# Optimization experiments

Measured on AMD Instinct MI355X. Metric: run time of the kernel, lower is better.

The kernel has to match this reference:

```python
import jax, jax.numpy as jnp
import numpy as np

N = 100000        # nodes
E = 1600000       # edges (avg degree 16)
IN_C = 128
HID = 128
OUT_C = 18


def setup_inputs() -> dict:
    key = jax.random.key(0)
    k_x, k_e, k_w1, k_b1, k_w2, k_b2 = jax.random.split(key, 6)
    x = jax.random.normal(k_x, (N, IN_C), dtype=jnp.float32)
    edge_index = jax.random.randint(k_e, (2, E), 0, N, dtype=jnp.int64)
    # Glorot-ish init for linear weights, zero bias (PyG GCNConv defaults)
    W1 = jax.random.normal(k_w1, (IN_C, HID), dtype=jnp.float32) / np.sqrt(IN_C)
    b1 = jnp.zeros((HID,), dtype=jnp.float32)
    W2 = jax.random.normal(k_w2, (HID, OUT_C), dtype=jnp.float32) / np.sqrt(HID)
    b2 = jnp.zeros((OUT_C,), dtype=jnp.float32)
    return {"x": x, "edge_index": edge_index, "W1": W1, "b1": b1, "W2": W2, "b2": b2}


def _gcn_conv(x, src, dst, norm, W, b, n_nodes):
    # PyG GCNConv: linear transform, then normalized scatter-add aggregation
    h = x @ W                                   # [N, d_out]
    msg = h[src] * norm[:, None]                # gather + scale: [E+N, d_out]
    out = jax.ops.segment_sum(msg, dst, num_segments=n_nodes)
    return out + b


def reference(x, edge_index, W1, b1, W2, b2):
    src, dst = edge_index[0], edge_index[1]
    loop = jnp.arange(N, dtype=edge_index.dtype)
    src_f = jnp.concatenate([src, loop])        # add self-loops
    dst_f = jnp.concatenate([dst, loop])
    # symmetric normalization deg^-1/2[src] * deg^-1/2[dst] (with self-loops)
    deg = jax.ops.segment_sum(jnp.ones_like(dst_f, dtype=x.dtype), dst_f, num_segments=N)
    dinv = jnp.where(deg > 0, jax.lax.rsqrt(deg), 0.0)
    norm = dinv[src_f] * dinv[dst_f]            # [E+N]

    h = _gcn_conv(x, src_f, dst_f, norm, W1, b1, N)
    h = jax.nn.relu(h)
    # dropout is identity in eval mode (training=False)
    h = _gcn_conv(h, src_f, dst_f, norm, W2, b2, N)
    return jax.nn.log_softmax(h, axis=1)
```

## Files before the change

kernel.cpp:

```cpp
#include <hip/hip_runtime.h>
#include <math.h>

#define NN 100000
#define NE 1600000
#define CH  128
#define CO  18
#define NPB 256
#define NBUK ((NN + NPB - 1) / NPB)
#define EPB 4096
#define NBB ((NE + EPB - 1) / EPB)

typedef unsigned int uint;
typedef unsigned short ushort;
typedef float floatx4 __attribute__((ext_vector_type(4)));
typedef short short8 __attribute__((ext_vector_type(8)));
typedef ushort ushort4v __attribute__((ext_vector_type(4)));

__device__ __forceinline__ float bf_lo(uint u) { return __uint_as_float(u << 16); }
__device__ __forceinline__ float bf_hi(uint u) { return __uint_as_float(u & 0xFFFF0000u); }
__device__ __forceinline__ ushort f2bf(float f) {
    uint u = __float_as_uint(f);
    u += 0x7FFFu + ((u >> 16) & 1u);
    return (ushort)(u >> 16);
}
__device__ __forceinline__ uint pack_bf16(float a, float b) {
    return (uint)f2bf(a) | ((uint)f2bf(b) << 16);
}


__global__ __launch_bounds__(256) void k_bhist(const int* __restrict__ dst,
                                               int* __restrict__ bcnt) {
    __shared__ int h[NBUK];
    int tid = threadIdx.x;
    for (int i = tid; i < NBUK; i += 256) h[i] = 0;
    __syncthreads();
    int e0 = blockIdx.x * EPB;
#pragma unroll
    for (int i = 0; i < EPB / 256; ++i) {
        int e = e0 + i * 256 + tid;
        if (e < NE) atomicAdd(&h[dst[e] >> 8], 1);
    }
    __syncthreads();
    for (int i = tid; i < NBUK; i += 256)
        if (h[i]) atomicAdd(&bcnt[i], h[i]);
}

__global__ __launch_bounds__(512) void k_bscan(const int* __restrict__ bcnt,
                                               int* __restrict__ bbase,
                                               int* __restrict__ bcur) {
    __shared__ int s[512];
    int tid = threadIdx.x;
    int c = (tid < NBUK) ? bcnt[tid] : 0;
    s[tid] = c;
    __syncthreads();
    for (int off = 1; off < 512; off <<= 1) {
        int t = (tid >= off) ? s[tid - off] : 0;
        __syncthreads();
        s[tid] += t;
        __syncthreads();
    }
    if (tid < NBUK) {
        int ex = s[tid] - c;
        bbase[tid] = ex;
        bcur[tid] = ex;
    }
    if (tid == NBUK) bbase[NBUK] = NE;
}

__global__ __launch_bounds__(256) void k_bin(const int* __restrict__ src,
                                             const int* __restrict__ dst,
                                             int* __restrict__ bcur,
                                             uint2* __restrict__ etmp) {
    __shared__ int h[NBUK];
    __shared__ int base[NBUK];
    int tid = threadIdx.x;
    for (int i = tid; i < NBUK; i += 256) h[i] = 0;
    __syncthreads();

    int e0 = blockIdx.x * EPB;
    int sv[EPB / 256], dv[EPB / 256];
#pragma unroll
    for (int i = 0; i < EPB / 256; ++i) {
        int e = e0 + i * 256 + tid;
        if (e < NE) {
            sv[i] = src[e];
            dv[i] = dst[e];
            atomicAdd(&h[dv[i] >> 8], 1);
        } else {
            dv[i] = -1;
        }
    }
    __syncthreads();
    for (int i = tid; i < NBUK; i += 256)
        base[i] = h[i] ? atomicAdd(&bcur[i], h[i]) : 0;
    __syncthreads();
    for (int i = tid; i < NBUK; i += 256) h[i] = 0;
    __syncthreads();
#pragma unroll
    for (int i = 0; i < EPB / 256; ++i) {
        if (dv[i] >= 0) {
            int b = dv[i] >> 8;
            int pos = base[b] + atomicAdd(&h[b], 1);
            etmp[pos] = make_uint2((uint)sv[i], (uint)dv[i]);
        }
    }
}

__global__ __launch_bounds__(256) void k_pass2(const int* __restrict__ bbase,
                                               const uint2* __restrict__ etmp,
                                               int* __restrict__ row_start,
                                               float* __restrict__ dinv,
                                               int* __restrict__ csr_src) {
    __shared__ int hist[NPB];
    __shared__ int s[NPB];
    __shared__ int cur[NPB];
    int tid = threadIdx.x;
    int b = blockIdx.x;
    int e0 = bbase[b], e1 = bbase[b + 1];

    hist[tid] = 0;
    __syncthreads();
    for (int e = e0 + tid; e < e1; e += 256)
        atomicAdd(&hist[etmp[e].y & 255], 1);
    __syncthreads();

    int c = hist[tid];
    s[tid] = c;
    __syncthreads();
    for (int off = 1; off < 256; off <<= 1) {
        int t = (tid >= off) ? s[tid - off] : 0;
        __syncthreads();
        s[tid] += t;
        __syncthreads();
    }
    int pfx = s[tid] - c;
    s[tid] = pfx;
    cur[tid] = 0;

    int node = b * NPB + tid;
    if (node < NN) {
        row_start[node] = e0 + pfx;
        dinv[node] = rsqrtf((float)c + 1.0f);
    }
    if (b == NBUK - 1 && tid == 0) row_start[NN] = NE;
    __syncthreads();

    for (int e = e0 + tid; e < e1; e += 256) {
        uint2 r = etmp[e];
        int n = r.y & 255;
        int p = e0 + s[n] + atomicAdd(&cur[n], 1);
        csr_src[p] = (int)r.x;
    }
}


__global__ __launch_bounds__(256) void k_wprep(const float* __restrict__ W1,
                                               ushort* __restrict__ Wt) {
    int t = blockIdx.x * 256 + threadIdx.x;
    if (t < 128 * 128) {
        int k = t >> 7, n = t & 127;
        Wt[n * 128 + k] = f2bf(W1[t]);
    }
}


__global__ __launch_bounds__(256, 2) void k_gemm1(const float* __restrict__ x,
                                                  const uint* __restrict__ Wtg,
                                                  ushort* __restrict__ h1s) {
    __shared__ ushort As[128 * 128];
    __shared__ ushort Bs[128 * 128];
    int tid = threadIdx.x;
    int row0 = blockIdx.x * 128;

    for (int i = 0; i < 32; ++i) {
        int j = i * 256 + tid;
        int n = j >> 6, ku = j & 63;
        int uidx = (n * 64 + ku) ^ ((n & 7) << 2);
        ((uint*)Bs)[uidx] = Wtg[j];
    }
    for (int i = 0; i < 16; ++i) {
        int flat = i * 256 + tid;
        int r = flat >> 5, c4 = flat & 31;
        int gr = row0 + r;
        float4 v = (gr < NN) ? ((const float4*)x)[(size_t)gr * 32 + c4]
                             : make_float4(0.f, 0.f, 0.f, 0.f);
        ushort4v p;
        p.x = f2bf(v.x); p.y = f2bf(v.y); p.z = f2bf(v.z); p.w = f2bf(v.w);
        int idx = (r * 128 + c4 * 4) ^ ((r & 7) << 3);
        *(ushort4v*)&As[idx] = p;
    }
    __syncthreads();

    int lane = tid & 63;
    int wave = tid >> 6;
    int wrow = wave * 32;
    int lr = lane & 15;
    int lk8 = (lane >> 4) * 8;

    floatx4 acc[2][8];
#pragma unroll
    for (int a = 0; a < 2; ++a)
#pragma unroll
        for (int b = 0; b < 8; ++b) acc[a][b] = (floatx4)(0.0f);

#pragma unroll
    for (int ks = 0; ks < 4; ++ks) {
        int k0 = ks * 32 + lk8;
        int r0r = wrow + lr;
        int r1r = wrow + 16 + lr;
        short8 a0 = *(const short8*)&As[(r0r * 128 + k0) ^ ((r0r & 7) << 3)];
        short8 a1 = *(const short8*)&As[(r1r * 128 + k0) ^ ((r1r & 7) << 3)];
#pragma unroll
        for (int nt = 0; nt < 8; ++nt) {
            int n = nt * 16 + lr;
            short8 bf = *(const short8*)&Bs[(n * 128 + k0) ^ ((n & 7) << 3)];
            acc[0][nt] = __builtin_amdgcn_mfma_f32_16x16x32_bf16(a0, bf, acc[0][nt], 0, 0, 0);
            acc[1][nt] = __builtin_amdgcn_mfma_f32_16x16x32_bf16(a1, bf, acc[1][nt], 0, 0, 0);
        }
    }

    int drow = (lane >> 4) * 4;
#pragma unroll
    for (int rt = 0; rt < 2; ++rt) {
#pragma unroll
        for (int i = 0; i < 4; ++i) {
            int gr = row0 + wrow + rt * 16 + drow + i;
            if (gr < NN) {
                size_t base = (size_t)gr * 128;
#pragma unroll
                for (int nt = 0; nt < 8; ++nt)
                    h1s[base + nt * 16 + lr] = f2bf(acc[rt][nt][i]);
            }
        }
    }
}


__global__ __launch_bounds__(256) void k_agg1(const int* __restrict__ row_start,
                                              const int* __restrict__ csr_src,
                                              const float* __restrict__ dinv,
                                              const uint* __restrict__ h1u,
                                              const float* __restrict__ b1,
                                              uint* __restrict__ h1ru) {
    int wave = threadIdx.x >> 6;
    int lane = threadIdx.x & 63;
    int i = blockIdx.x * 4 + wave;
    if (i >= NN) return;
    int r0 = row_start[i], r1 = row_start[i + 1];
    float di = dinv[i];
    float ax = 0.0f, ay = 0.0f;

    int j = r0;
    for (; j + 3 < r1; j += 4) {
        int s0 = csr_src[j], s1 = csr_src[j + 1];
        int s2 = csr_src[j + 2], s3 = csr_src[j + 3];
        float w0 = dinv[s0] * di, w1 = dinv[s1] * di;
        float w2 = dinv[s2] * di, w3 = dinv[s3] * di;
        uint u0 = h1u[(size_t)s0 * 64 + lane];
        uint u1 = h1u[(size_t)s1 * 64 + lane];
        uint u2 = h1u[(size_t)s2 * 64 + lane];
        uint u3 = h1u[(size_t)s3 * 64 + lane];
        ax += w0 * bf_lo(u0) + w1 * bf_lo(u1) + w2 * bf_lo(u2) + w3 * bf_lo(u3);
        ay += w0 * bf_hi(u0) + w1 * bf_hi(u1) + w2 * bf_hi(u2) + w3 * bf_hi(u3);
    }
    for (; j < r1; ++j) {
        int s0 = csr_src[j];
        float w0 = dinv[s0] * di;
        uint u0 = h1u[(size_t)s0 * 64 + lane];
        ax += w0 * bf_lo(u0);
        ay += w0 * bf_hi(u0);
    }

    uint us = h1u[(size_t)i * 64 + lane];
    float2 bb = ((const float2*)b1)[lane];
    float di2 = di * di;
    float ox = fmaxf(ax + di2 * bf_lo(us) + bb.x, 0.0f);
    float oy = fmaxf(ay + di2 * bf_hi(us) + bb.y, 0.0f);
    h1ru[(size_t)i * 64 + lane] = pack_bf16(ox, oy);
}


__global__ __launch_bounds__(256, 2) void k_gemm2(const uint* __restrict__ h1ru,
                                                  const float* __restrict__ W2,
                                                  ushort* __restrict__ h2b) {
    __shared__ float xs[128][129];
    __shared__ float Ws[128 * 18];
    int row0 = blockIdx.x * 128;
    int tid = threadIdx.x;

    for (int i = tid; i < 128 * 18; i += 256) Ws[i] = W2[i];
    for (int i = tid; i < 128 * 64; i += 256) {
        int r = i >> 6, c2 = i & 63;
        int gr = row0 + r;
        uint u = (gr < NN) ? h1ru[(size_t)gr * 64 + c2] : 0u;
        xs[r][2 * c2]     = bf_lo(u);
        xs[r][2 * c2 + 1] = bf_hi(u);
    }
    __syncthreads();

    int rl   = tid & 127;
    int half = tid >> 7;
    int j0   = half * 9;
    float acc[9];
#pragma unroll
    for (int j = 0; j < 9; ++j) acc[j] = 0.0f;

#pragma unroll 4
    for (int k = 0; k < 128; ++k) {
        float xv = xs[rl][k];
#pragma unroll
        for (int j = 0; j < 9; ++j)
            acc[j] += xv * Ws[k * 18 + j0 + j];
    }
    int gr = row0 + rl;
    if (gr < NN) {
#pragma unroll
        for (int j = 0; j < 9; ++j)
            h2b[(size_t)gr * 18 + j0 + j] = f2bf(acc[j]);
    }
}


__global__ __launch_bounds__(256) void k_agg2(const int* __restrict__ row_start,
                                              const int* __restrict__ csr_src,
                                              const float* __restrict__ dinv,
                                              const uint* __restrict__ h2u,
                                              const float* __restrict__ b2,
                                              float* __restrict__ out) {
    int i = blockIdx.x * 256 + threadIdx.x;
    if (i >= NN) return;
    int r0 = row_start[i], r1 = row_start[i + 1];
    float di = dinv[i];
    float acc[CO];
#pragma unroll
    for (int j = 0; j < CO; ++j) acc[j] = 0.0f;

    for (int e = r0; e < r1; ++e) {
        int s = csr_src[e];
        float w = dinv[s] * di;
        const uint* hr = h2u + (size_t)s * 9;
#pragma unroll
        for (int j = 0; j < 9; ++j) {
            uint u = hr[j];
            acc[2 * j]     += w * bf_lo(u);
            acc[2 * j + 1] += w * bf_hi(u);
        }
    }

    float di2 = di * di;
    const uint* hi = h2u + (size_t)i * 9;
    float m = -1e30f;
#pragma unroll
    for (int j = 0; j < 9; ++j) {
        uint u = hi[j];
        acc[2 * j]     += di2 * bf_lo(u) + b2[2 * j];
        acc[2 * j + 1] += di2 * bf_hi(u) + b2[2 * j + 1];
    }
#pragma unroll
    for (int j = 0; j < CO; ++j) m = fmaxf(m, acc[j]);
    float sum = 0.0f;
#pragma unroll
    for (int j = 0; j < CO; ++j) sum += expf(acc[j] - m);
    float lse = logf(sum);
    float* op = out + (size_t)i * CO;
#pragma unroll
    for (int j = 0; j < CO; ++j) op[j] = acc[j] - m - lse;
}


extern "C" void kernel_launch(void* const* d_in, const int* in_sizes, int n_in,
                              void* d_out, int out_size, void* d_ws, size_t ws_size,
                              hipStream_t stream) {
    const float* x  = (const float*)d_in[0];
    const int*   ei = (const int*)d_in[1];
    const float* W1 = (const float*)d_in[2];
    const float* b1 = (const float*)d_in[3];
    const float* W2 = (const float*)d_in[4];
    const float* b2 = (const float*)d_in[5];
    float* out = (float*)d_out;

    const int* src = ei;
    const int* dst = ei + NE;

    uint* h1u  = (uint*)d_ws;
    uint* h1ru = h1u + (size_t)NN * 64;
    uint* h2u  = h1ru + (size_t)NN * 64;
    float* dinv = (float*)(h2u + (size_t)NN * 9);
    int* row_start = (int*)(dinv + NN);
    int* csr_src   = row_start + NN + 1;
    uint2* etmp    = (uint2*)(csr_src + NE);
    int* bcnt      = (int*)(etmp + NE);
    int* bbase     = bcnt + NBUK;
    int* bcur      = bbase + NBUK + 1;
    ushort* Wt     = (ushort*)(bcur + NBUK);

    hipMemsetAsync(bcnt, 0, NBUK * sizeof(int), stream);

    k_bhist<<<NBB, 256, 0, stream>>>(dst, bcnt);
    k_bscan<<<1, 512, 0, stream>>>(bcnt, bbase, bcur);
    k_bin<<<NBB, 256, 0, stream>>>(src, dst, bcur, etmp);
    k_pass2<<<NBUK, 256, 0, stream>>>(bbase, etmp, row_start, dinv, csr_src);

    k_wprep<<<64, 256, 0, stream>>>(W1, Wt);
    k_gemm1<<<(NN + 127) / 128, 256, 0, stream>>>(x, (const uint*)Wt, (ushort*)h1u);
    k_agg1<<<(NN + 3) / 4, 256, 0, stream>>>(row_start, csr_src, dinv, h1u, b1, h1ru);
    k_gemm2<<<(NN + 127) / 128, 256, 0, stream>>>(h1ru, W2, (ushort*)h2u);
    k_agg2<<<(NN + 255) / 256, 256, 0, stream>>>(row_start, csr_src, dinv, h2u, b2, out);
}
```

Baseline: 250.2 us.

## Fuse layer-1 aggregation with layer-2 MFMA GEMM and pack binned edges

Merges the first-layer neighbor aggregation with the second linear transform. Each 128-row block aggregates its rows into LDS as bf16 and then runs a bf16 MFMA GEMM against a padded, transposed W2 prepared in k_wprep. This avoids writing and re-reading the intermediate h1 activation and replaces the scalar fp32 GEMM. The binning temp array is also packed from uint2 to a single uint (src<<8 | local dst), which halves that traffic. In exchange, the fused kernel has far fewer waves in flight for the latency-bound gather (782 blocks, each wave doing 32 rows serially), and the gather loop is unrolled to 8 to compensate.

```diff
diff --git a/kernel.cpp b/kernel.cpp
--- a/kernel.cpp
+++ b/kernel.cpp
@@ -70,7 +70,7 @@
 __global__ __launch_bounds__(256) void k_bin(const int* __restrict__ src,
                                              const int* __restrict__ dst,
                                              int* __restrict__ bcur,
-                                             uint2* __restrict__ etmp) {
+                                             uint* __restrict__ etmp) {
     __shared__ int h[NBUK];
     __shared__ int base[NBUK];
     int tid = threadIdx.x;
@@ -101,13 +101,13 @@
         if (dv[i] >= 0) {
             int b = dv[i] >> 8;
             int pos = base[b] + atomicAdd(&h[b], 1);
-            etmp[pos] = make_uint2((uint)sv[i], (uint)dv[i]);
+            etmp[pos] = ((uint)sv[i] << 8) | ((uint)dv[i] & 255u);
         }
     }
 }
 
 __global__ __launch_bounds__(256) void k_pass2(const int* __restrict__ bbase,
-                                               const uint2* __restrict__ etmp,
+                                               const uint* __restrict__ etmp,
                                                int* __restrict__ row_start,
                                                float* __restrict__ dinv,
                                                int* __restrict__ csr_src) {
@@ -121,7 +121,7 @@
     hist[tid] = 0;
     __syncthreads();
     for (int e = e0 + tid; e < e1; e += 256)
-        atomicAdd(&hist[etmp[e].y & 255], 1);
+        atomicAdd(&hist[etmp[e] & 255u], 1);
     __syncthreads();
 
     int c = hist[tid];
@@ -146,20 +146,26 @@
     __syncthreads();
 
     for (int e = e0 + tid; e < e1; e += 256) {
-        uint2 r = etmp[e];
-        int n = r.y & 255;
+        uint r = etmp[e];
+        int n = (int)(r & 255u);
         int p = e0 + s[n] + atomicAdd(&cur[n], 1);
-        csr_src[p] = (int)r.x;
+        csr_src[p] = (int)(r >> 8);
     }
 }
 
 
 __global__ __launch_bounds__(256) void k_wprep(const float* __restrict__ W1,
-                                               ushort* __restrict__ Wt) {
+                                               const float* __restrict__ W2,
+                                               ushort* __restrict__ Wt,
+                                               ushort* __restrict__ W2t) {
     int t = blockIdx.x * 256 + threadIdx.x;
     if (t < 128 * 128) {
         int k = t >> 7, n = t & 127;
         Wt[n * 128 + k] = f2bf(W1[t]);
+    }
+    if (t < 32 * 128) {
+        int n = t >> 7, k = t & 127;
+        W2t[t] = (n < CO) ? f2bf(W2[k * CO + n]) : (ushort)0;
     }
 }
 
@@ -236,87 +242,113 @@
 }
 
 
-__global__ __launch_bounds__(256) void k_agg1(const int* __restrict__ row_start,
-                                              const int* __restrict__ csr_src,
-                                              const float* __restrict__ dinv,
-                                              const uint* __restrict__ h1u,
-                                              const float* __restrict__ b1,
-                                              uint* __restrict__ h1ru) {
-    int wave = threadIdx.x >> 6;
-    int lane = threadIdx.x & 63;
-    int i = blockIdx.x * 4 + wave;
-    if (i >= NN) return;
-    int r0 = row_start[i], r1 = row_start[i + 1];
-    float di = dinv[i];
-    float ax = 0.0f, ay = 0.0f;
-
-    int j = r0;
-    for (; j + 3 < r1; j += 4) {
-        int s0 = csr_src[j], s1 = csr_src[j + 1];
-        int s2 = csr_src[j + 2], s3 = csr_src[j + 3];
-        float w0 = dinv[s0] * di, w1 = dinv[s1] * di;
-        float w2 = dinv[s2] * di, w3 = dinv[s3] * di;
-        uint u0 = h1u[(size_t)s0 * 64 + lane];
-        uint u1 = h1u[(size_t)s1 * 64 + lane];
-        uint u2 = h1u[(size_t)s2 * 64 + lane];
-        uint u3 = h1u[(size_t)s3 * 64 + lane];
-        ax += w0 * bf_lo(u0) + w1 * bf_lo(u1) + w2 * bf_lo(u2) + w3 * bf_lo(u3);
-        ay += w0 * bf_hi(u0) + w1 * bf_hi(u1) + w2 * bf_hi(u2) + w3 * bf_hi(u3);
-    }
-    for (; j < r1; ++j) {
-        int s0 = csr_src[j];
-        float w0 = dinv[s0] * di;
-        uint u0 = h1u[(size_t)s0 * 64 + lane];
-        ax += w0 * bf_lo(u0);
-        ay += w0 * bf_hi(u0);
-    }
-
-    uint us = h1u[(size_t)i * 64 + lane];
+__global__ __launch_bounds__(256, 2) void k_agg1_gemm2(
+        const int* __restrict__ row_start, const int* __restrict__ csr_src,
+        const float* __restrict__ dinv, const uint* __restrict__ h1u,
+        const float* __restrict__ b1, const uint* __restrict__ W2tg,
+        ushort* __restrict__ h2b) {
+    __shared__ ushort As[128 * 128];
+    __shared__ ushort Bs[32 * 128];
+    int tid = threadIdx.x;
+    int lane = tid & 63;
+    int wave = tid >> 6;
+    int row0 = blockIdx.x * 128;
+
+    for (int j = tid; j < 2048; j += 256) {
+        int n = j >> 6, ku = j & 63;
+        ((uint*)Bs)[(n * 64 + ku) ^ ((n & 7) << 2)] = W2tg[j];
+    }
+
     float2 bb = ((const float2*)b1)[lane];
-    float di2 = di * di;
-    float ox = fmaxf(ax + di2 * bf_lo(us) + bb.x, 0.0f);
-    float oy = fmaxf(ay + di2 * bf_hi(us) + bb.y, 0.0f);
-    h1ru[(size_t)i * 64 + lane] = pack_bf16(ox, oy);
-}
-
-
-__global__ __launch_bounds__(256, 2) void k_gemm2(const uint* __restrict__ h1ru,
-                                                  const float* __restrict__ W2,
-                                                  ushort* __restrict__ h2b) {
-    __shared__ float xs[128][129];
-    __shared__ float Ws[128 * 18];
-    int row0 = blockIdx.x * 128;
-    int tid = threadIdx.x;
-
-    for (int i = tid; i < 128 * 18; i += 256) Ws[i] = W2[i];
-    for (int i = tid; i < 128 * 64; i += 256) {
-        int r = i >> 6, c2 = i & 63;
-        int gr = row0 + r;
-        uint u = (gr < NN) ? h1ru[(size_t)gr * 64 + c2] : 0u;
-        xs[r][2 * c2]     = bf_lo(u);
-        xs[r][2 * c2 + 1] = bf_hi(u);
-    }
-    __syncthreads();
-
-    int rl   = tid & 127;
-    int half = tid >> 7;
-    int j0   = half * 9;
-    float acc[9];
-#pragma unroll
-    for (int j = 0; j < 9; ++j) acc[j] = 0.0f;
-
-#pragma unroll 4
-    for (int k = 0; k < 128; ++k) {
-        float xv = xs[rl][k];
-#pragma unroll
-        for (int j = 0; j < 9; ++j)
-            acc[j] += xv * Ws[k * 18 + j0 + j];
-    }
-    int gr = row0 + rl;
-    if (gr < NN) {
-#pragma unroll
-        for (int j = 0; j < 9; ++j)
-            h2b[(size_t)gr * 18 + j0 + j] = f2bf(acc[j]);
+
+    for (int t = 0; t < 32; ++t) {
+        int r = wave * 32 + t;
+        int i = row0 + r;
+        uint outv = 0u;
+        if (i < NN) {
+            int r0 = row_start[i], r1 = row_start[i + 1];
+            float di = dinv[i];
+            float ax = 0.0f, ay = 0.0f;
+            int j = r0;
+            for (; j + 7 < r1; j += 8) {
+                int s0 = csr_src[j],     s1 = csr_src[j + 1];
+                int s2 = csr_src[j + 2], s3 = csr_src[j + 3];
+                int s4 = csr_src[j + 4], s5 = csr_src[j + 5];
+                int s6 = csr_src[j + 6], s7 = csr_src[j + 7];
+                float w0 = dinv[s0] * di, w1 = dinv[s1] * di;
+                float w2 = dinv[s2] * di, w3 = dinv[s3] * di;
+                float w4 = dinv[s4] * di, w5 = dinv[s5] * di;
+                float w6 = dinv[s6] * di, w7 = dinv[s7] * di;
+                uint u0 = h1u[(size_t)s0 * 64 + lane];
+                uint u1 = h1u[(size_t)s1 * 64 + lane];
+                uint u2 = h1u[(size_t)s2 * 64 + lane];
+                uint u3 = h1u[(size_t)s3 * 64 + lane];
+                uint u4 = h1u[(size_t)s4 * 64 + lane];
+                uint u5 = h1u[(size_t)s5 * 64 + lane];
+                uint u6 = h1u[(size_t)s6 * 64 + lane];
+                uint u7 = h1u[(size_t)s7 * 64 + lane];
+                ax += w0 * bf_lo(u0) + w1 * bf_lo(u1) + w2 * bf_lo(u2) + w3 * bf_lo(u3)
+                    + w4 * bf_lo(u4) + w5 * bf_lo(u5) + w6 * bf_lo(u6) + w7 * bf_lo(u7);
+                ay += w0 * bf_hi(u0) + w1 * bf_hi(u1) + w2 * bf_hi(u2) + w3 * bf_hi(u3)
+                    + w4 * bf_hi(u4) + w5 * bf_hi(u5) + w6 * bf_hi(u6) + w7 * bf_hi(u7);
+            }
+            for (; j < r1; ++j) {
+                int s0 = csr_src[j];
+                float w0 = dinv[s0] * di;
+                uint u0 = h1u[(size_t)s0 * 64 + lane];
+                ax += w0 * bf_lo(u0);
+                ay += w0 * bf_hi(u0);
+            }
+            uint us = h1u[(size_t)i * 64 + lane];
+            float di2 = di * di;
+            float ox = fmaxf(ax + di2 * bf_lo(us) + bb.x, 0.0f);
+            float oy = fmaxf(ay + di2 * bf_hi(us) + bb.y, 0.0f);
+            outv = pack_bf16(ox, oy);
+        }
+        *(uint*)&As[(r * 128 + lane * 2) ^ ((r & 7) << 3)] = outv;
+    }
+    __syncthreads();
+
+    int lr = lane & 15;
+    int lk8 = (lane >> 4) * 8;
+    int wrow = wave * 32;
+    floatx4 acc[2][2];
+#pragma unroll
+    for (int a = 0; a < 2; ++a)
+#pragma unroll
+        for (int b = 0; b < 2; ++b) acc[a][b] = (floatx4)(0.0f);
+
+#pragma unroll
+    for (int ks = 0; ks < 4; ++ks) {
+        int k0 = ks * 32 + lk8;
+        int r0r = wrow + lr;
+        int r1r = wrow + 16 + lr;
+        short8 a0 = *(const short8*)&As[(r0r * 128 + k0) ^ ((r0r & 7) << 3)];
+        short8 a1 = *(const short8*)&As[(r1r * 128 + k0) ^ ((r1r & 7) << 3)];
+#pragma unroll
+        for (int nt = 0; nt < 2; ++nt) {
+            int n = nt * 16 + lr;
+            short8 bf = *(const short8*)&Bs[(n * 128 + k0) ^ ((n & 7) << 3)];
+            acc[0][nt] = __builtin_amdgcn_mfma_f32_16x16x32_bf16(a0, bf, acc[0][nt], 0, 0, 0);
+            acc[1][nt] = __builtin_amdgcn_mfma_f32_16x16x32_bf16(a1, bf, acc[1][nt], 0, 0, 0);
+        }
+    }
+
+    int drow = (lane >> 4) * 4;
+#pragma unroll
+    for (int rt = 0; rt < 2; ++rt) {
+#pragma unroll
+        for (int i = 0; i < 4; ++i) {
+            int gr = row0 + wrow + rt * 16 + drow + i;
+            if (gr < NN) {
+#pragma unroll
+                for (int nt = 0; nt < 2; ++nt) {
+                    int col = nt * 16 + lr;
+                    if (col < CO)
+                        h2b[(size_t)gr * CO + col] = f2bf(acc[rt][nt][i]);
+                }
+            }
+        }
     }
 }
 
@@ -383,16 +415,16 @@
     const int* dst = ei + NE;
 
     uint* h1u  = (uint*)d_ws;
-    uint* h1ru = h1u + (size_t)NN * 64;
-    uint* h2u  = h1ru + (size_t)NN * 64;
+    uint* h2u  = h1u + (size_t)NN * 64;
     float* dinv = (float*)(h2u + (size_t)NN * 9);
     int* row_start = (int*)(dinv + NN);
     int* csr_src   = row_start + NN + 1;
-    uint2* etmp    = (uint2*)(csr_src + NE);
+    uint* etmp     = (uint*)(csr_src + NE);
     int* bcnt      = (int*)(etmp + NE);
     int* bbase     = bcnt + NBUK;
     int* bcur      = bbase + NBUK + 1;
     ushort* Wt     = (ushort*)(bcur + NBUK);
+    ushort* W2t    = Wt + 128 * 128;
 
     hipMemsetAsync(bcnt, 0, NBUK * sizeof(int), stream);
 
@@ -401,9 +433,10 @@
     k_bin<<<NBB, 256, 0, stream>>>(src, dst, bcur, etmp);
     k_pass2<<<NBUK, 256, 0, stream>>>(bbase, etmp, row_start, dinv, csr_src);
 
-    k_wprep<<<64, 256, 0, stream>>>(W1, Wt);
+    k_wprep<<<64, 256, 0, stream>>>(W1, W2, Wt, W2t);
     k_gemm1<<<(NN + 127) / 128, 256, 0, stream>>>(x, (const uint*)Wt, (ushort*)h1u);
-    k_agg1<<<(NN + 3) / 4, 256, 0, stream>>>(row_start, csr_src, dinv, h1u, b1, h1ru);
-    k_gemm2<<<(NN + 127) / 128, 256, 0, stream>>>(h1ru, W2, (ushort*)h2u);
+    k_agg1_gemm2<<<(NN + 127) / 128, 256, 0, stream>>>(row_start, csr_src, dinv,
+                                                       h1u, b1, (const uint*)W2t,
+                                                       (ushort*)h2u);
     k_agg2<<<(NN + 255) / 256, 256, 0, stream>>>(row_start, csr_src, dinv, h2u, b2, out);
 }
```

Measured after the change: 272.4 us. 1.09x slower.

## Pack binned edges, pad layer-2 rows to 48 bytes, unroll gathers deeper

Applied to the files above, without the earlier changes.

Binned edges are packed into one 32-bit word (source shifted left by 8, local destination in the low byte), which halves the temporary traffic in the CSR build. The layer-2 hidden rows are padded from 36 to 48 bytes so each row can be read with two 16-byte loads plus one word, and the layer-2 aggregation is unrolled by 4 edges. The layer-1 gather is unrolled from 4 to 8 edges to keep more loads in flight. The packing needs source indices below 2^24, the padding adds workspace and write bytes, and the deeper unrolls raise register pressure.

```diff
diff --git a/kernel.cpp b/kernel.cpp
--- a/kernel.cpp
+++ b/kernel.cpp
@@ -70,7 +70,7 @@
 __global__ __launch_bounds__(256) void k_bin(const int* __restrict__ src,
                                              const int* __restrict__ dst,
                                              int* __restrict__ bcur,
-                                             uint2* __restrict__ etmp) {
+                                             uint* __restrict__ etmp) {
     __shared__ int h[NBUK];
     __shared__ int base[NBUK];
     int tid = threadIdx.x;
@@ -101,13 +101,13 @@
         if (dv[i] >= 0) {
             int b = dv[i] >> 8;
             int pos = base[b] + atomicAdd(&h[b], 1);
-            etmp[pos] = make_uint2((uint)sv[i], (uint)dv[i]);
+            etmp[pos] = ((uint)sv[i] << 8) | ((uint)dv[i] & 255u);
         }
     }
 }
 
 __global__ __launch_bounds__(256) void k_pass2(const int* __restrict__ bbase,
-                                               const uint2* __restrict__ etmp,
+                                               const uint* __restrict__ etmp,
                                                int* __restrict__ row_start,
                                                float* __restrict__ dinv,
                                                int* __restrict__ csr_src) {
@@ -121,7 +121,7 @@
     hist[tid] = 0;
     __syncthreads();
     for (int e = e0 + tid; e < e1; e += 256)
-        atomicAdd(&hist[etmp[e].y & 255], 1);
+        atomicAdd(&hist[etmp[e] & 255u], 1);
     __syncthreads();
 
     int c = hist[tid];
@@ -146,10 +146,10 @@
     __syncthreads();
 
     for (int e = e0 + tid; e < e1; e += 256) {
-        uint2 r = etmp[e];
-        int n = r.y & 255;
+        uint r = etmp[e];
+        int n = (int)(r & 255u);
         int p = e0 + s[n] + atomicAdd(&cur[n], 1);
-        csr_src[p] = (int)r.x;
+        csr_src[p] = (int)(r >> 8);
     }
 }
 
@@ -251,17 +251,27 @@
     float ax = 0.0f, ay = 0.0f;
 
     int j = r0;
-    for (; j + 3 < r1; j += 4) {
-        int s0 = csr_src[j], s1 = csr_src[j + 1];
+    for (; j + 7 < r1; j += 8) {
+        int s0 = csr_src[j],     s1 = csr_src[j + 1];
         int s2 = csr_src[j + 2], s3 = csr_src[j + 3];
+        int s4 = csr_src[j + 4], s5 = csr_src[j + 5];
+        int s6 = csr_src[j + 6], s7 = csr_src[j + 7];
         float w0 = dinv[s0] * di, w1 = dinv[s1] * di;
         float w2 = dinv[s2] * di, w3 = dinv[s3] * di;
+        float w4 = dinv[s4] * di, w5 = dinv[s5] * di;
+        float w6 = dinv[s6] * di, w7 = dinv[s7] * di;
         uint u0 = h1u[(size_t)s0 * 64 + lane];
         uint u1 = h1u[(size_t)s1 * 64 + lane];
         uint u2 = h1u[(size_t)s2 * 64 + lane];
         uint u3 = h1u[(size_t)s3 * 64 + lane];
-        ax += w0 * bf_lo(u0) + w1 * bf_lo(u1) + w2 * bf_lo(u2) + w3 * bf_lo(u3);
-        ay += w0 * bf_hi(u0) + w1 * bf_hi(u1) + w2 * bf_hi(u2) + w3 * bf_hi(u3);
+        uint u4 = h1u[(size_t)s4 * 64 + lane];
+        uint u5 = h1u[(size_t)s5 * 64 + lane];
+        uint u6 = h1u[(size_t)s6 * 64 + lane];
+        uint u7 = h1u[(size_t)s7 * 64 + lane];
+        ax += w0 * bf_lo(u0) + w1 * bf_lo(u1) + w2 * bf_lo(u2) + w3 * bf_lo(u3)
+            + w4 * bf_lo(u4) + w5 * bf_lo(u5) + w6 * bf_lo(u6) + w7 * bf_lo(u7);
+        ay += w0 * bf_hi(u0) + w1 * bf_hi(u1) + w2 * bf_hi(u2) + w3 * bf_hi(u3)
+            + w4 * bf_hi(u4) + w5 * bf_hi(u5) + w6 * bf_hi(u6) + w7 * bf_hi(u7);
     }
     for (; j < r1; ++j) {
         int s0 = csr_src[j];
@@ -316,10 +326,23 @@
     if (gr < NN) {
 #pragma unroll
         for (int j = 0; j < 9; ++j)
-            h2b[(size_t)gr * 18 + j0 + j] = f2bf(acc[j]);
-    }
-}
-
+            h2b[(size_t)gr * 24 + j0 + j] = f2bf(acc[j]);
+    }
+}
+
+
+__device__ __forceinline__ void acc_row(float* acc, float w,
+                                        uint4 a, uint4 b, uint c) {
+    acc[0]  += w * bf_lo(a.x); acc[1]  += w * bf_hi(a.x);
+    acc[2]  += w * bf_lo(a.y); acc[3]  += w * bf_hi(a.y);
+    acc[4]  += w * bf_lo(a.z); acc[5]  += w * bf_hi(a.z);
+    acc[6]  += w * bf_lo(a.w); acc[7]  += w * bf_hi(a.w);
+    acc[8]  += w * bf_lo(b.x); acc[9]  += w * bf_hi(b.x);
+    acc[10] += w * bf_lo(b.y); acc[11] += w * bf_hi(b.y);
+    acc[12] += w * bf_lo(b.z); acc[13] += w * bf_hi(b.z);
+    acc[14] += w * bf_lo(b.w); acc[15] += w * bf_hi(b.w);
+    acc[16] += w * bf_lo(c);   acc[17] += w * bf_hi(c);
+}
 
 __global__ __launch_bounds__(256) void k_agg2(const int* __restrict__ row_start,
                                               const int* __restrict__ csr_src,
@@ -335,29 +358,44 @@
 #pragma unroll
     for (int j = 0; j < CO; ++j) acc[j] = 0.0f;
 
-    for (int e = r0; e < r1; ++e) {
+    int e = r0;
+    for (; e + 3 < r1; e += 4) {
+        int s0 = csr_src[e],     s1 = csr_src[e + 1];
+        int s2 = csr_src[e + 2], s3 = csr_src[e + 3];
+        float w0 = dinv[s0] * di, w1 = dinv[s1] * di;
+        float w2 = dinv[s2] * di, w3 = dinv[s3] * di;
+        const uint4* p0 = (const uint4*)(h2u + (size_t)s0 * 12);
+        const uint4* p1 = (const uint4*)(h2u + (size_t)s1 * 12);
+        const uint4* p2 = (const uint4*)(h2u + (size_t)s2 * 12);
+        const uint4* p3 = (const uint4*)(h2u + (size_t)s3 * 12);
+        uint4 a0 = p0[0], b0 = p0[1]; uint c0 = ((const uint*)p0)[8];
+        uint4 a1 = p1[0], b1v = p1[1]; uint c1 = ((const uint*)p1)[8];
+        uint4 a2 = p2[0], b2v = p2[1]; uint c2 = ((const uint*)p2)[8];
+        uint4 a3 = p3[0], b3v = p3[1]; uint c3 = ((const uint*)p3)[8];
+        acc_row(acc, w0, a0, b0, c0);
+        acc_row(acc, w1, a1, b1v, c1);
+        acc_row(acc, w2, a2, b2v, c2);
+        acc_row(acc, w3, a3, b3v, c3);
+    }
+    for (; e < r1; ++e) {
         int s = csr_src[e];
         float w = dinv[s] * di;
-        const uint* hr = h2u + (size_t)s * 9;
-#pragma unroll
-        for (int j = 0; j < 9; ++j) {
-            uint u = hr[j];
-            acc[2 * j]     += w * bf_lo(u);
-            acc[2 * j + 1] += w * bf_hi(u);
-        }
+        const uint4* p = (const uint4*)(h2u + (size_t)s * 12);
+        uint4 a = p[0], b = p[1]; uint c = ((const uint*)p)[8];
+        acc_row(acc, w, a, b, c);
     }
 
     float di2 = di * di;
-    const uint* hi = h2u + (size_t)i * 9;
+    const uint4* pi = (const uint4*)(h2u + (size_t)i * 12);
+    uint4 ia = pi[0], ib = pi[1]; uint ic = ((const uint*)pi)[8];
+    acc_row(acc, di2, ia, ib, ic);
+
     float m = -1e30f;
 #pragma unroll
-    for (int j = 0; j < 9; ++j) {
-        uint u = hi[j];
-        acc[2 * j]     += di2 * bf_lo(u) + b2[2 * j];
-        acc[2 * j + 1] += di2 * bf_hi(u) + b2[2 * j + 1];
-    }
-#pragma unroll
-    for (int j = 0; j < CO; ++j) m = fmaxf(m, acc[j]);
+    for (int j = 0; j < CO; ++j) {
+        acc[j] += b2[j];
+        m = fmaxf(m, acc[j]);
+    }
     float sum = 0.0f;
 #pragma unroll
     for (int j = 0; j < CO; ++j) sum += expf(acc[j] - m);
@@ -385,10 +423,10 @@
     uint* h1u  = (uint*)d_ws;
     uint* h1ru = h1u + (size_t)NN * 64;
     uint* h2u  = h1ru + (size_t)NN * 64;
-    float* dinv = (float*)(h2u + (size_t)NN * 9);
+    float* dinv = (float*)(h2u + (size_t)NN * 12);
     int* row_start = (int*)(dinv + NN);
     int* csr_src   = row_start + NN + 1;
-    uint2* etmp    = (uint2*)(csr_src + NE);
+    uint* etmp     = (uint*)(csr_src + NE);
     int* bcnt      = (int*)(etmp + NE);
     int* bbase     = bcnt + NBUK;
     int* bcur      = bbase + NBUK + 1;
```

Measured after the change: 247.0 us. About the same (-1.3%).
